# Performance work log

Hardware: AMD Instinct MI355X
Metric: run time of the kernel (lower is better)

The kernel has to match this reference:

```python
import jax, jax.numpy as jnp
import numpy as np

NUM_HEADS = 12  # per init_kwargs


def setup_inputs() -> dict:
    key = jax.random.key(0)
    k1, k2, k3 = jax.random.split(key, 3)
    B, H, W, D = 1, 64, 64, 768
    x = jax.random.normal(k1, (B, H, W, D), dtype=jnp.float32)
    # torch nn.Linear weights are [out, in]; small init keeps softmax well-conditioned
    w_qkv = jax.random.normal(k2, (3 * D, D), dtype=jnp.float32) * 0.02
    w_proj = jax.random.normal(k3, (D, D), dtype=jnp.float32) * 0.02
    b_proj = jnp.zeros((D,), dtype=jnp.float32)
    return {"x": x, "w_qkv": w_qkv, "w_proj": w_proj, "b_proj": b_proj}


def reference(x, w_qkv, w_proj, b_proj):
    B, H, W, D = x.shape
    S = H * W
    nh = NUM_HEADS
    hd = D // nh
    scale = hd ** (-0.5)
    # qkv: [B, S, 3, nh, hd] -> q,k,v each [B, nh, S, hd]
    qkv = jnp.einsum('bhwd,ed->bhwe', x, w_qkv).reshape(B, S, 3, nh, hd)
    qkv = jnp.transpose(qkv, (2, 0, 3, 1, 4))
    q, k, v = qkv[0], qkv[1], qkv[2]
    # full O(S^2) attention matrix, as in the original module
    wei = jnp.einsum('bnqd,bnkd->bnqk', q * scale, k)
    wei = jax.nn.softmax(wei, axis=-1)
    # att_drop omitted (eval mode / deterministic baseline)
    out = jnp.einsum('bnqk,bnkd->bnqd', wei, v)  # [B, nh, S, hd]
    # [B, nh, H, W, hd] -> [B, H, W, nh*hd]
    out = jnp.transpose(out.reshape(B, nh, H, W, hd), (0, 2, 3, 1, 4)).reshape(B, H, W, D)
    proj = jnp.einsum('bhwd,ed->bhwe', out, w_proj) + b_proj
    return proj
```

## Files before the change

kernel.cpp:

```cpp
#include <hip/hip_runtime.h>
#include <hip/hip_bf16.h>
#include <math.h>

typedef short s16x8 __attribute__((ext_vector_type(8)));
typedef float f32x4 __attribute__((ext_vector_type(4)));
typedef __hip_bfloat16 bf16;

#define GLD16(g, l)                                                        \
  __builtin_amdgcn_global_load_lds(                                        \
      (const __attribute__((address_space(1))) void*)(g),                  \
      (__attribute__((address_space(3))) void*)(l), 16, 0, 0)

#define MFMA16(a, b, c) __builtin_amdgcn_mfma_f32_16x16x32_bf16((a), (b), (c), 0, 0, 0)

static constexpr int kS = 4096;
static constexpr int kD = 768;
static constexpr int kNH = 12;
static constexpr int kHD = 64;
static constexpr int kNE = 2304;

static constexpr int kNX8 = kS * kD / 8;
static constexpr int kNWq8 = kNE * kD / 8;
static constexpr int kNWp8 = kD * kD / 8;

__global__ __launch_bounds__(256)
void k_cvt3(const float* __restrict__ x, const float* __restrict__ wq,
            const float* __restrict__ wp, bf16* __restrict__ xb,
            bf16* __restrict__ wqb, bf16* __restrict__ wpb) {
  int i = blockIdx.x * 256 + threadIdx.x;
  const float* src;
  short* dst;
  if (i < kNX8) {
    src = x; dst = (short*)xb;
  } else if (i < kNX8 + kNWq8) {
    i -= kNX8; src = wq; dst = (short*)wqb;
  } else {
    i -= kNX8 + kNWq8; if (i >= kNWp8) return;
    src = wp; dst = (short*)wpb;
  }
  const f32x4 a = *(const f32x4*)(src + i * 8);
  const f32x4 b = *(const f32x4*)(src + i * 8 + 4);
  s16x8 o;
#pragma unroll
  for (int j = 0; j < 4; ++j) {
    o[j] = (short)__bfloat16_as_ushort(__float2bfloat16(a[j]));
    o[j + 4] = (short)__bfloat16_as_ushort(__float2bfloat16(b[j]));
  }
  *(s16x8*)(dst + i * 8) = o;
}

__global__ __launch_bounds__(256, 2)
void k_qkv(const bf16* __restrict__ X, const bf16* __restrict__ W,
           bf16* __restrict__ Qw, bf16* __restrict__ Kw, bf16* __restrict__ Vw) {
  __shared__ __align__(16) short As[2][128 * 32];
  __shared__ __align__(16) short Bs[2][128 * 32];
  const int tid = threadIdx.x;
  const int wv = tid >> 6, ln = tid & 63;
  const int r = ln & 15, kq = ln >> 4;
  const int bm = blockIdx.x * 128;
  const int bn = blockIdx.y * 128;
  const int wr = wv >> 1, wc = wv & 1;
  const short* Xs = (const short*)X;
  const short* Ws = (const short*)W;

  f32x4 acc[4][4] = {};

  const int c0 = wv * 128 + ln, c1 = c0 + 64;
  const int ra0 = c0 >> 2, ka0 = c0 & 3;
  const int ra1 = c1 >> 2, ka1 = c1 & 3;
  const int off0 = wv * 1024, off1 = off0 + 512;
  const short* gA0 = Xs + (bm + ra0) * kD + ka0 * 8;
  const short* gA1 = Xs + (bm + ra1) * kD + ka1 * 8;
  const short* gB0 = Ws + (bn + ra0) * kD + ka0 * 8;
  const short* gB1 = Ws + (bn + ra1) * kD + ka1 * 8;

  GLD16(gA0, &As[0][off0]);
  GLD16(gA1, &As[0][off1]);
  GLD16(gB0, &Bs[0][off0]);
  GLD16(gB1, &Bs[0][off1]);
  __syncthreads();

  const int NT = kD / 32;
  for (int t = 0; t < NT; ++t) {
    const short* aCur = As[t & 1];
    const short* bCur = Bs[t & 1];
    if (t + 1 < NT) {
      const int k1 = (t + 1) * 32;
      short* aN = As[(t + 1) & 1];
      short* bN = Bs[(t + 1) & 1];
      GLD16(gA0 + k1, aN + off0);
      GLD16(gA1 + k1, aN + off1);
      GLD16(gB0 + k1, bN + off0);
      GLD16(gB1 + k1, bN + off1);
    }
    s16x8 a[4], b[4];
#pragma unroll
    for (int i = 0; i < 4; ++i)
      a[i] = *(const s16x8*)(aCur + (wr * 64 + i * 16 + r) * 32 + kq * 8);
#pragma unroll
    for (int j = 0; j < 4; ++j)
      b[j] = *(const s16x8*)(bCur + (wc * 64 + j * 16 + r) * 32 + kq * 8);
#pragma unroll
    for (int i = 0; i < 4; ++i)
#pragma unroll
      for (int j = 0; j < 4; ++j) acc[i][j] = MFMA16(a[i], b[j], acc[i][j]);
    __syncthreads();
  }

  const int which = bn / kD;
  bf16* dst = (which == 0) ? Qw : (which == 1) ? Kw : Vw;
  const float scl = (which == 0) ? 0.125f * 1.44269504088896f : 1.0f;
  const int ebase = bn - which * kD + wc * 64;
#pragma unroll
  for (int j = 0; j < 4; ++j) {
    const int e = ebase + j * 16 + r;
    const int h = e >> 6, d = e & 63;
#pragma unroll
    for (int i = 0; i < 4; ++i) {
      const int srow = bm + wr * 64 + i * 16 + kq * 4;
#pragma unroll
      for (int rr = 0; rr < 4; ++rr)
        dst[(h * kS + srow + rr) * kHD + d] = __float2bfloat16(acc[i][j][rr] * scl);
    }
  }
}

__global__ __launch_bounds__(256, 2)
void k_vt(const bf16* __restrict__ Vw, bf16* __restrict__ Vt) {
  __shared__ __align__(16) short L[64 * 72];
  const int h = blockIdx.y, st = blockIdx.x;
  const int t = threadIdx.x;
  const short* src = (const short*)Vw + (h * kS + st * 64) * kHD;
  short* dstb = (short*)Vt + h * kHD * kS;
#pragma unroll
  for (int u = 0; u < 2; ++u) {
    const int c = u * 256 + t;
    const int row = c >> 3, ch = c & 7;
    *(s16x8*)(L + row * 72 + ch * 8) = *(const s16x8*)(src + row * kHD + ch * 8);
  }
  __syncthreads();
#pragma unroll
  for (int u = 0; u < 2; ++u) {
    const int c = u * 256 + t;
    const int d = c >> 3, ch = c & 7;
    s16x8 v;
#pragma unroll
    for (int j = 0; j < 8; ++j) v[j] = L[(ch * 8 + j) * 72 + d];
    *(s16x8*)(dstb + d * kS + st * 64 + ch * 8) = v;
  }
}

__global__ __launch_bounds__(256, 3)
void k_attn(const bf16* __restrict__ Qw, const bf16* __restrict__ Kw,
            const bf16* __restrict__ Vt, bf16* __restrict__ Att) {
  __shared__ __align__(16) short Ks[2][64 * 64];
  __shared__ __align__(16) short Vs[2][64 * 64];
  __shared__ __align__(16) bf16 Ps[4][16][72];
  const int tid = threadIdx.x;
  const int wv = tid >> 6, ln = tid & 63;
  const int r = ln & 15, kq = ln >> 4;
  const int h = blockIdx.y;
  const int q0 = blockIdx.x * 64;
  const short* Qh = (const short*)Qw + (h * kS + q0) * kHD;
  const short* Kh = (const short*)Kw + h * kS * kHD;
  const short* Vh = (const short*)Vt + h * kHD * kS;

  s16x8 aq[2];
#pragma unroll
  for (int ks = 0; ks < 2; ++ks)
    aq[ks] = *(const s16x8*)(Qh + (wv * 16 + r) * kHD + ks * 32 + kq * 8);

  f32x4 o[4] = {};
  float lp[4] = {0.f, 0.f, 0.f, 0.f};

  const int c0 = wv * 128 + ln, c1 = c0 + 64;
  const int kr0 = c0 >> 3, g0 = (c0 & 7) ^ (kr0 & 7);
  const int kr1 = c1 >> 3, g1 = (c1 & 7) ^ (kr1 & 7);
  const int off0 = wv * 1024, off1 = off0 + 512;
  const short* gK0 = Kh + kr0 * kHD + g0 * 8;
  const short* gK1 = Kh + kr1 * kHD + g1 * 8;
  const short* gV0 = Vh + kr0 * kS + g0 * 8;
  const short* gV1 = Vh + kr1 * kS + g1 * 8;

  GLD16(gK0, &Ks[0][off0]);
  GLD16(gK1, &Ks[0][off1]);
  GLD16(gV0, &Vs[0][off0]);
  GLD16(gV1, &Vs[0][off1]);
  __syncthreads();

  const int NT = kS / 64;
  for (int kt = 0; kt < NT; ++kt) {
    const short* ksCur = Ks[kt & 1];
    const short* vsCur = Vs[kt & 1];
    if (kt + 1 < NT) {
      short* ksN = Ks[(kt + 1) & 1];
      short* vsN = Vs[(kt + 1) & 1];
      const int dk = (kt + 1) * 64 * kHD;
      const int dv = (kt + 1) * 64;
      GLD16(gK0 + dk, ksN + off0);
      GLD16(gK1 + dk, ksN + off1);
      GLD16(gV0 + dv, vsN + off0);
      GLD16(gV1 + dv, vsN + off1);
    }

    f32x4 sf[4];
    __builtin_amdgcn_s_setprio(1);
#pragma unroll
    for (int nt = 0; nt < 4; ++nt) {
      const int R = nt * 16 + r;
      const int sw = R & 7;
      s16x8 b0 = *(const s16x8*)(ksCur + R * 64 + ((kq) ^ sw) * 8);
      s16x8 b1 = *(const s16x8*)(ksCur + R * 64 + ((kq + 4) ^ sw) * 8);
      f32x4 z = {};
      z = MFMA16(aq[0], b0, z);
      z = MFMA16(aq[1], b1, z);
      sf[nt] = z;
    }
    __builtin_amdgcn_s_setprio(0);

#pragma unroll
    for (int nt = 0; nt < 4; ++nt) {
#pragma unroll
      for (int rr = 0; rr < 4; ++rr) {
        const float p = exp2f(sf[nt][rr]);
        lp[rr] += p;
        Ps[wv][kq * 4 + rr][nt * 16 + r] = __float2bfloat16(p);
      }
    }
    asm volatile("s_waitcnt lgkmcnt(0)" ::: "memory");

    s16x8 pa0 = *(const s16x8*)&Ps[wv][r][kq * 8];
    s16x8 pa1 = *(const s16x8*)&Ps[wv][r][32 + kq * 8];
    __builtin_amdgcn_s_setprio(1);
#pragma unroll
    for (int nt = 0; nt < 4; ++nt) {
      const int R = nt * 16 + r;
      const int sw = R & 7;
      s16x8 v0 = *(const s16x8*)(vsCur + R * 64 + ((kq) ^ sw) * 8);
      s16x8 v1 = *(const s16x8*)(vsCur + R * 64 + ((kq + 4) ^ sw) * 8);
      o[nt] = MFMA16(pa0, v0, o[nt]);
      o[nt] = MFMA16(pa1, v1, o[nt]);
    }
    __builtin_amdgcn_s_setprio(0);
    __syncthreads();
  }

  float inv[4];
#pragma unroll
  for (int rr = 0; rr < 4; ++rr) {
    float v = lp[rr];
    v += __shfl_xor(v, 1);
    v += __shfl_xor(v, 2);
    v += __shfl_xor(v, 4);
    v += __shfl_xor(v, 8);
    inv[rr] = 1.0f / v;
  }
#pragma unroll
  for (int nt = 0; nt < 4; ++nt) {
    const int d = nt * 16 + r;
#pragma unroll
    for (int rr = 0; rr < 4; ++rr) {
      const int srow = q0 + wv * 16 + kq * 4 + rr;
      Att[srow * kD + h * kHD + d] = __float2bfloat16(o[nt][rr] * inv[rr]);
    }
  }
}

__global__ __launch_bounds__(256, 3)
void k_proj(const bf16* __restrict__ A, const bf16* __restrict__ W,
            const float* __restrict__ Bias, float* __restrict__ Out) {
  __shared__ __align__(16) short As[2][64 * 32];
  __shared__ __align__(16) short Bs[2][64 * 32];
  const int tid = threadIdx.x;
  const int wv = tid >> 6, ln = tid & 63;
  const int r = ln & 15, kq = ln >> 4;
  const int bm = blockIdx.x * 64;
  const int bn = blockIdx.y * 64;
  const int wr = wv >> 1, wc = wv & 1;
  const short* Asrc = (const short*)A;
  const short* Wsrc = (const short*)W;

  f32x4 acc[2][2] = {};
  const int c = wv * 64 + ln;
  const int ra = c >> 2, ka = c & 3;
  const int off = wv * 512;
  const short* gA = Asrc + (bm + ra) * kD + ka * 8;
  const short* gB = Wsrc + (bn + ra) * kD + ka * 8;

  GLD16(gA, &As[0][off]);
  GLD16(gB, &Bs[0][off]);
  __syncthreads();

  const int NT = kD / 32;
  for (int t = 0; t < NT; ++t) {
    const short* aCur = As[t & 1];
    const short* bCur = Bs[t & 1];
    if (t + 1 < NT) {
      const int k1 = (t + 1) * 32;
      GLD16(gA + k1, &As[(t + 1) & 1][off]);
      GLD16(gB + k1, &Bs[(t + 1) & 1][off]);
    }
    s16x8 a[2], b[2];
#pragma unroll
    for (int i = 0; i < 2; ++i)
      a[i] = *(const s16x8*)(aCur + (wr * 32 + i * 16 + r) * 32 + kq * 8);
#pragma unroll
    for (int j = 0; j < 2; ++j)
      b[j] = *(const s16x8*)(bCur + (wc * 32 + j * 16 + r) * 32 + kq * 8);
#pragma unroll
    for (int i = 0; i < 2; ++i)
#pragma unroll
      for (int j = 0; j < 2; ++j) acc[i][j] = MFMA16(a[i], b[j], acc[i][j]);
    __syncthreads();
  }
#pragma unroll
  for (int j = 0; j < 2; ++j) {
    const int e = bn + wc * 32 + j * 16 + r;
    const float bv = Bias[e];
#pragma unroll
    for (int i = 0; i < 2; ++i) {
      const int srow = bm + wr * 32 + i * 16 + kq * 4;
#pragma unroll
      for (int rr = 0; rr < 4; ++rr)
        Out[(srow + rr) * kD + e] = acc[i][j][rr] + bv;
    }
  }
}

extern "C" void kernel_launch(void* const* d_in, const int* in_sizes, int n_in,
                              void* d_out, int out_size, void* d_ws, size_t ws_size,
                              hipStream_t stream) {
  const float* x = (const float*)d_in[0];
  const float* w_qkv = (const float*)d_in[1];
  const float* w_proj = (const float*)d_in[2];
  const float* b_proj = (const float*)d_in[3];
  float* out = (float*)d_out;

  const size_t HS = (size_t)kNH * kS * kHD;
  const int nX = kS * kD;
  const int nWq = kNE * kD;
  const int nWp = kD * kD;

  bf16* Xb = (bf16*)d_ws;
  bf16* Wqb = Xb + nX;
  bf16* Wpb = Wqb + nWq;
  bf16* Qw = Wpb + nWp;
  bf16* Kw = Qw + HS;
  bf16* Vw = Kw + HS;
  bf16* Vt = Vw + HS;
  bf16* At = Vt + HS;

  const int totalC = kNX8 + kNWq8 + kNWp8;
  k_cvt3<<<(totalC + 255) / 256, 256, 0, stream>>>(x, w_qkv, w_proj, Xb, Wqb, Wpb);

  k_qkv<<<dim3(kS / 128, kNE / 128), 256, 0, stream>>>(Xb, Wqb, Qw, Kw, Vw);
  k_vt<<<dim3(kS / 64, kNH), 256, 0, stream>>>(Vw, Vt);
  k_attn<<<dim3(kS / 64, kNH), 256, 0, stream>>>(Qw, Kw, Vt, At);
  k_proj<<<dim3(kS / 64, kD / 64), 256, 0, stream>>>(At, Wpb, b_proj, out);
}
```

Baseline: 158.4 us.

## Rewrite attention with 32x32 MFMA, transposed scores and register-resident P

The attention kernel now computes S^T = K·Q^T with 32x32x16 bf16 MFMAs, two waves per block each owning 32 queries. P is repacked in registers with a cross-half lane shuffle instead of going through an LDS scratch buffer. exp2 with a folded log2e factor is replaced by __expf. This removes the LDS round-trip and wait for P and uses the larger MFMA shape. In exchange, blocks are half as wide (128 threads), so each block loads K/V tiles with fewer waves, and the kernel still has no running-max subtraction.

```diff
diff --git a/kernel.cpp b/kernel.cpp
--- a/kernel.cpp
+++ b/kernel.cpp
@@ -4,6 +4,7 @@
 
 typedef short s16x8 __attribute__((ext_vector_type(8)));
 typedef float f32x4 __attribute__((ext_vector_type(4)));
+typedef float f32x16 __attribute__((ext_vector_type(16)));
 typedef __hip_bfloat16 bf16;
 
 #define GLD16(g, l)                                                        \
@@ -12,6 +13,7 @@
       (__attribute__((address_space(3))) void*)(l), 16, 0, 0)
 
 #define MFMA16(a, b, c) __builtin_amdgcn_mfma_f32_16x16x32_bf16((a), (b), (c), 0, 0, 0)
+#define MFMA32(a, b, c) __builtin_amdgcn_mfma_f32_32x32x16_bf16((a), (b), (c), 0, 0, 0)
 
 static constexpr int kS = 4096;
 static constexpr int kD = 768;
@@ -109,7 +111,7 @@
 
   const int which = bn / kD;
   bf16* dst = (which == 0) ? Qw : (which == 1) ? Kw : Vw;
-  const float scl = (which == 0) ? 0.125f * 1.44269504088896f : 1.0f;
+  const float scl = (which == 0) ? 0.125f : 1.0f;
   const int ebase = bn - which * kD + wc * 64;
 #pragma unroll
   for (int j = 0; j < 4; ++j) {
@@ -150,42 +152,46 @@
   }
 }
 
-__global__ __launch_bounds__(256, 3)
+__global__ __launch_bounds__(128, 2)
 void k_attn(const bf16* __restrict__ Qw, const bf16* __restrict__ Kw,
             const bf16* __restrict__ Vt, bf16* __restrict__ Att) {
   __shared__ __align__(16) short Ks[2][64 * 64];
   __shared__ __align__(16) short Vs[2][64 * 64];
-  __shared__ __align__(16) bf16 Ps[4][16][72];
   const int tid = threadIdx.x;
   const int wv = tid >> 6, ln = tid & 63;
-  const int r = ln & 15, kq = ln >> 4;
-  const int h = blockIdx.y;
+  const int col = ln & 31;
+  const int lh = ln >> 5;
+  const int hh = blockIdx.y;
   const int q0 = blockIdx.x * 64;
-  const short* Qh = (const short*)Qw + (h * kS + q0) * kHD;
-  const short* Kh = (const short*)Kw + h * kS * kHD;
-  const short* Vh = (const short*)Vt + h * kHD * kS;
-
-  s16x8 aq[2];
-#pragma unroll
-  for (int ks = 0; ks < 2; ++ks)
-    aq[ks] = *(const s16x8*)(Qh + (wv * 16 + r) * kHD + ks * 32 + kq * 8);
-
-  f32x4 o[4] = {};
-  float lp[4] = {0.f, 0.f, 0.f, 0.f};
-
-  const int c0 = wv * 128 + ln, c1 = c0 + 64;
-  const int kr0 = c0 >> 3, g0 = (c0 & 7) ^ (kr0 & 7);
-  const int kr1 = c1 >> 3, g1 = (c1 & 7) ^ (kr1 & 7);
-  const int off0 = wv * 1024, off1 = off0 + 512;
-  const short* gK0 = Kh + kr0 * kHD + g0 * 8;
-  const short* gK1 = Kh + kr1 * kHD + g1 * 8;
-  const short* gV0 = Vh + kr0 * kS + g0 * 8;
-  const short* gV1 = Vh + kr1 * kS + g1 * 8;
-
-  GLD16(gK0, &Ks[0][off0]);
-  GLD16(gK1, &Ks[0][off1]);
-  GLD16(gV0, &Vs[0][off0]);
-  GLD16(gV1, &Vs[0][off1]);
+  const short* Qh = (const short*)Qw + ((size_t)hh * kS + q0 + wv * 32) * kHD;
+  const short* Kh = (const short*)Kw + (size_t)hh * kS * kHD;
+  const short* Vh = (const short*)Vt + (size_t)hh * kHD * kS;
+
+  s16x8 bq[4];
+#pragma unroll
+  for (int kb = 0; kb < 4; ++kb)
+    bq[kb] = *(const s16x8*)(Qh + col * kHD + kb * 16 + lh * 8);
+
+  f32x16 o[2] = {};
+  float lp = 0.f;
+
+  int ldso[4];
+  const short* gK[4];
+  const short* gV[4];
+#pragma unroll
+  for (int u = 0; u < 4; ++u) {
+    const int c = u * 128 + tid;
+    const int kr = c >> 3, g = (c & 7) ^ (kr & 7);
+    ldso[u] = c * 8;
+    gK[u] = Kh + kr * kHD + g * 8;
+    gV[u] = Vh + kr * kS + g * 8;
+  }
+
+#pragma unroll
+  for (int u = 0; u < 4; ++u) {
+    GLD16(gK[u], &Ks[0][ldso[u]]);
+    GLD16(gV[u], &Vs[0][ldso[u]]);
+  }
   __syncthreads();
 
   const int NT = kS / 64;
@@ -197,73 +203,84 @@
       short* vsN = Vs[(kt + 1) & 1];
       const int dk = (kt + 1) * 64 * kHD;
       const int dv = (kt + 1) * 64;
-      GLD16(gK0 + dk, ksN + off0);
-      GLD16(gK1 + dk, ksN + off1);
-      GLD16(gV0 + dv, vsN + off0);
-      GLD16(gV1 + dv, vsN + off1);
-    }
-
-    f32x4 sf[4];
-    __builtin_amdgcn_s_setprio(1);
-#pragma unroll
-    for (int nt = 0; nt < 4; ++nt) {
-      const int R = nt * 16 + r;
-      const int sw = R & 7;
-      s16x8 b0 = *(const s16x8*)(ksCur + R * 64 + ((kq) ^ sw) * 8);
-      s16x8 b1 = *(const s16x8*)(ksCur + R * 64 + ((kq + 4) ^ sw) * 8);
-      f32x4 z = {};
-      z = MFMA16(aq[0], b0, z);
-      z = MFMA16(aq[1], b1, z);
-      sf[nt] = z;
-    }
-    __builtin_amdgcn_s_setprio(0);
-
-#pragma unroll
-    for (int nt = 0; nt < 4; ++nt) {
-#pragma unroll
-      for (int rr = 0; rr < 4; ++rr) {
-        const float p = exp2f(sf[nt][rr]);
-        lp[rr] += p;
-        Ps[wv][kq * 4 + rr][nt * 16 + r] = __float2bfloat16(p);
-      }
-    }
-    asm volatile("s_waitcnt lgkmcnt(0)" ::: "memory");
-
-    s16x8 pa0 = *(const s16x8*)&Ps[wv][r][kq * 8];
-    s16x8 pa1 = *(const s16x8*)&Ps[wv][r][32 + kq * 8];
-    __builtin_amdgcn_s_setprio(1);
-#pragma unroll
-    for (int nt = 0; nt < 4; ++nt) {
-      const int R = nt * 16 + r;
-      const int sw = R & 7;
-      s16x8 v0 = *(const s16x8*)(vsCur + R * 64 + ((kq) ^ sw) * 8);
-      s16x8 v1 = *(const s16x8*)(vsCur + R * 64 + ((kq + 4) ^ sw) * 8);
-      o[nt] = MFMA16(pa0, v0, o[nt]);
-      o[nt] = MFMA16(pa1, v1, o[nt]);
-    }
-    __builtin_amdgcn_s_setprio(0);
+#pragma unroll
+      for (int u = 0; u < 4; ++u) {
+        GLD16(gK[u] + dk, ksN + ldso[u]);
+        GLD16(gV[u] + dv, vsN + ldso[u]);
+      }
+    }
+
+#pragma unroll
+    for (int kvb = 0; kvb < 2; ++kvb) {
+      f32x16 z = {};
+      const int krow = kvb * 32 + col;
+      const int ksw = krow & 7;
+      __builtin_amdgcn_s_setprio(1);
+#pragma unroll
+      for (int kb = 0; kb < 4; ++kb) {
+        const int ch = ((kb << 1) + lh) ^ ksw;
+        s16x8 ak = *(const s16x8*)(ksCur + krow * 64 + ch * 8);
+        z = MFMA32(ak, bq[kb], z);
+      }
+      __builtin_amdgcn_s_setprio(0);
+
+      float p[16];
+#pragma unroll
+      for (int g = 0; g < 16; ++g) {
+        p[g] = __expf(z[g]);
+        lp += p[g];
+      }
+      unsigned own[8], oth[8];
+#pragma unroll
+      for (int m = 0; m < 4; ++m) {
+        own[2 * m] = (unsigned)__bfloat16_as_ushort(__float2bfloat16(p[4 * m])) |
+                     ((unsigned)__bfloat16_as_ushort(__float2bfloat16(p[4 * m + 1])) << 16);
+        own[2 * m + 1] = (unsigned)__bfloat16_as_ushort(__float2bfloat16(p[4 * m + 2])) |
+                         ((unsigned)__bfloat16_as_ushort(__float2bfloat16(p[4 * m + 3])) << 16);
+      }
+#pragma unroll
+      for (int i = 0; i < 8; ++i) oth[i] = __shfl_xor(own[i], 32);
+
+      __builtin_amdgcn_s_setprio(1);
+#pragma unroll
+      for (int kvk = 0; kvk < 2; ++kvk) {
+        const int m = 2 * kvk + lh;
+        union { unsigned u[4]; s16x8 v; } ap;
+        ap.u[0] = lh ? oth[2 * m] : own[2 * m];
+        ap.u[1] = lh ? oth[2 * m + 1] : own[2 * m + 1];
+        ap.u[2] = lh ? own[2 * m] : oth[2 * m];
+        ap.u[3] = lh ? own[2 * m + 1] : oth[2 * m + 1];
+        const int kvg = kvb * 2 + kvk;
+#pragma unroll
+        for (int db = 0; db < 2; ++db) {
+          const int vrow = db * 32 + col;
+          const int ch = ((kvg << 1) + lh) ^ (vrow & 7);
+          s16x8 vb = *(const s16x8*)(vsCur + vrow * 64 + ch * 8);
+          o[db] = MFMA32(ap.v, vb, o[db]);
+        }
+      }
+      __builtin_amdgcn_s_setprio(0);
+    }
     __syncthreads();
   }
 
-  float inv[4];
-#pragma unroll
-  for (int rr = 0; rr < 4; ++rr) {
-    float v = lp[rr];
-    v += __shfl_xor(v, 1);
-    v += __shfl_xor(v, 2);
-    v += __shfl_xor(v, 4);
-    v += __shfl_xor(v, 8);
-    inv[rr] = 1.0f / v;
-  }
-#pragma unroll
-  for (int nt = 0; nt < 4; ++nt) {
-    const int d = nt * 16 + r;
-#pragma unroll
-    for (int rr = 0; rr < 4; ++rr) {
-      const int srow = q0 + wv * 16 + kq * 4 + rr;
-      Att[srow * kD + h * kHD + d] = __float2bfloat16(o[nt][rr] * inv[rr]);
-    }
-  }
+  lp += __shfl_xor(lp, 32);
+  const float inv = 1.0f / lp;
+  float invq[16];
+#pragma unroll
+  for (int g = 0; g < 16; ++g) {
+    const int qoff = (g & 3) + 8 * (g >> 2) + 4 * lh;
+    invq[g] = __shfl(inv, qoff);
+  }
+#pragma unroll
+  for (int db = 0; db < 2; ++db)
+#pragma unroll
+    for (int g = 0; g < 16; ++g) {
+      const int qoff = (g & 3) + 8 * (g >> 2) + 4 * lh;
+      const int srow = q0 + wv * 32 + qoff;
+      Att[srow * kD + hh * kHD + db * 32 + col] =
+          __float2bfloat16(o[db][g] * invq[g]);
+    }
 }
 
 __global__ __launch_bounds__(256, 3)
@@ -355,6 +372,6 @@
 
   k_qkv<<<dim3(kS / 128, kNE / 128), 256, 0, stream>>>(Xb, Wqb, Qw, Kw, Vw);
   k_vt<<<dim3(kS / 64, kNH), 256, 0, stream>>>(Vw, Vt);
-  k_attn<<<dim3(kS / 64, kNH), 256, 0, stream>>>(Qw, Kw, Vt, At);
+  k_attn<<<dim3(kS / 64, kNH), 128, 0, stream>>>(Qw, Kw, Vt, At);
   k_proj<<<dim3(kS / 64, kD / 64), 256, 0, stream>>>(At, Wpb, b_proj, out);
 }
```

Result: slower. 230.1 us (+45.2%).
